# Performance work log

Measured on AMD Instinct MI355X. Metric: run time of the kernel, lower is better.

## Reference

```python
import jax, jax.numpy as jnp
import numpy as np

D_MODEL = 2048
HEADS = 16
HEAD_DIM = D_MODEL // HEADS
INNER = 8192
SEQ = 2048
EPS = 1e-5


def _layernorm(x, g, b):
    mu = jnp.mean(x, axis=-1, keepdims=True)
    var = jnp.mean(jnp.square(x - mu), axis=-1, keepdims=True)
    return (x - mu) * jax.lax.rsqrt(var + EPS) * g + b


def setup_inputs() -> dict:
    key = jax.random.key(0)
    ks = jax.random.split(key, 10)
    s = 0.02
    return {
        "x": jax.random.normal(ks[0], (1, SEQ, D_MODEL), dtype=jnp.float32),
        "C_w": jax.random.normal(ks[1], (D_MODEL, 3 * D_MODEL), dtype=jnp.float32) * s,
        "C_b": jnp.zeros((3 * D_MODEL,), dtype=jnp.float32),
        "lin_w": jax.random.normal(ks[2], (D_MODEL, D_MODEL), dtype=jnp.float32) * s,
        "lin_b": jnp.zeros((D_MODEL,), dtype=jnp.float32),
        "ff1_w": jax.random.normal(ks[3], (D_MODEL, INNER), dtype=jnp.float32) * s,
        "ff1_b": jnp.zeros((INNER,), dtype=jnp.float32),
        "ff2_w": jax.random.normal(ks[4], (INNER, D_MODEL), dtype=jnp.float32) * s,
        "ff2_b": jnp.zeros((D_MODEL,), dtype=jnp.float32),
        "ln1_g": jnp.ones((D_MODEL,), dtype=jnp.float32),
        "ln1_b": jnp.zeros((D_MODEL,), dtype=jnp.float32),
        "ln2_g": jnp.ones((D_MODEL,), dtype=jnp.float32),
        "ln2_b": jnp.zeros((D_MODEL,), dtype=jnp.float32),
    }


def reference(x, C_w, C_b, lin_w, lin_b, ff1_w, ff1_b, ff2_w, ff2_b,
              ln1_g, ln1_b, ln2_g, ln2_b):
    b, s, d = x.shape
    c = x @ C_w + C_b                       # [b, s, 3d]
    q, k, v = jnp.split(c, 3, axis=2)
    q = q.reshape(b, s, HEADS, HEAD_DIM)
    k = k.reshape(b, s, HEADS, HEAD_DIM)
    v = v.reshape(b, s, HEADS, HEAD_DIM)
    # NOTE: source scales by sqrt(d_model), NOT sqrt(head_dim)
    qk = jnp.einsum('bqhd,bkhd->bhqk', q, k) / jnp.sqrt(jnp.float32(d))
    causal = jnp.tril(jnp.ones((s, s), dtype=bool))  # [s, s]
    qk = jnp.where(causal[None, None, :, :], qk, -jnp.inf)
    scores = jax.nn.softmax(qk, axis=3)
    out = jnp.einsum('bhqk,bkhd->bqhd', scores, v).reshape(b, s, d)
    attn = out @ lin_w + lin_b
    h1 = _layernorm(x + attn, ln1_g, ln1_b)
    ff = jax.nn.gelu(h1 @ ff1_w + ff1_b, approximate=False) @ ff2_w + ff2_b
    return _layernorm(h1 + ff, ln2_g, ln2_b)
```

## Files before the change

kernel.cpp:

```cpp
#include <hip/hip_runtime.h>
#include <hip/hip_bf16.h>

#define SEQ 2048
#define DM 2048
#define NH 16
#define HD 128
#define FF 8192

typedef float f4v __attribute__((ext_vector_type(4)));
typedef short s8v __attribute__((ext_vector_type(8)));

__device__ __forceinline__ ushort f2bf(float f) {
  unsigned int x = __float_as_uint(f);
  unsigned int r = (x + 0x7FFFu + ((x >> 16) & 1u)) >> 16;
  return (ushort)r;
}

__global__ __launch_bounds__(256) void k_cvt(const float* __restrict__ in,
                                             ushort* __restrict__ out, int n4) {
  int i = blockIdx.x * 256 + threadIdx.x;
  if (i >= n4) return;
  f4v v = reinterpret_cast<const f4v*>(in)[i];
  ushort4 u;
  u.x = f2bf(v[0]); u.y = f2bf(v[1]); u.z = f2bf(v[2]); u.w = f2bf(v[3]);
  reinterpret_cast<ushort4*>(out)[i] = u;
}

__global__ __launch_bounds__(256) void k_tr(const float* __restrict__ W,
                                            ushort* __restrict__ Wt,
                                            int K, int N) {
  __shared__ float tile[32][33];
  int tx = threadIdx.x & 31, ty = threadIdx.x >> 5;
  int n0 = blockIdx.x * 32, k0 = blockIdx.y * 32;
#pragma unroll
  for (int i = 0; i < 4; ++i)
    tile[ty + i * 8][tx] = W[(size_t)(k0 + ty + i * 8) * N + n0 + tx];
  __syncthreads();
#pragma unroll
  for (int i = 0; i < 4; ++i)
    Wt[(size_t)(n0 + ty + i * 8) * K + k0 + tx] = f2bf(tile[tx][ty + i * 8]);
}

__global__ __launch_bounds__(256) void k_gemm(const ushort* __restrict__ A,
                                              const ushort* __restrict__ Bt,
                                              const float* __restrict__ bias,
                                              float* __restrict__ Cf,
                                              ushort* __restrict__ Cb,
                                              int M, int N, int K, int gelu) {
  __shared__ ushort As[128][72];
  __shared__ ushort Bs[128][72];
  int m0 = blockIdx.y * 128, n0 = blockIdx.x * 128;
  int t = threadIdx.x;
  int wave = t >> 6, lane = t & 63;
  int wm = (wave >> 1) * 64, wn = (wave & 1) * 64;
  int quad = lane >> 4, l16 = lane & 15;
  f4v acc[4][4] = {};
  int srow = t >> 3, scol = (t & 7) * 8;
  for (int k0 = 0; k0 < K; k0 += 64) {
#pragma unroll
    for (int p = 0; p < 4; ++p) {
      int r = srow + p * 32;
      *(uint4*)&As[r][scol] = *(const uint4*)&A[(size_t)(m0 + r) * K + k0 + scol];
      *(uint4*)&Bs[r][scol] = *(const uint4*)&Bt[(size_t)(n0 + r) * K + k0 + scol];
    }
    __syncthreads();
#pragma unroll
    for (int kk = 0; kk < 64; kk += 32) {
      s8v af[4], bf[4];
#pragma unroll
      for (int i = 0; i < 4; ++i)
        af[i] = *(const s8v*)&As[wm + i * 16 + l16][kk + quad * 8];
#pragma unroll
      for (int j = 0; j < 4; ++j)
        bf[j] = *(const s8v*)&Bs[wn + j * 16 + l16][kk + quad * 8];
#pragma unroll
      for (int i = 0; i < 4; ++i)
#pragma unroll
        for (int j = 0; j < 4; ++j)
          acc[i][j] = __builtin_amdgcn_mfma_f32_16x16x32_bf16(af[i], bf[j], acc[i][j], 0, 0, 0);
    }
    __syncthreads();
  }
#pragma unroll
  for (int i = 0; i < 4; ++i) {
    int rbase = m0 + wm + i * 16 + quad * 4;
#pragma unroll
    for (int j = 0; j < 4; ++j) {
      int cidx = n0 + wn + j * 16 + l16;
      float b = bias[cidx];
#pragma unroll
      for (int r = 0; r < 4; ++r) {
        float v = acc[i][j][r] + b;
        if (gelu) v = 0.5f * v * (1.0f + erff(v * 0.70710678118654752f));
        if (Cf) Cf[(size_t)(rbase + r) * N + cidx] = v;
        if (Cb) Cb[(size_t)(rbase + r) * N + cidx] = f2bf(v);
      }
    }
  }
}

__global__ __launch_bounds__(256) void k_attn_mfma(const ushort* __restrict__ qkv,
                                                   ushort* __restrict__ ctx) {
  __shared__ ushort Ks[64][136];
  __shared__ ushort Vt[128][72];
  __shared__ ushort Ps[4][16][72];
  const int idx = blockIdx.x;
  const int h = idx & (NH - 1);
  const int qt = (SEQ / 64 - 1) - (idx >> 4);
  const int q0 = qt * 64;
  const int t = threadIdx.x;
  const int wave = t >> 6, lane = t & 63;
  const int quad = lane >> 4, l16 = lane & 15;
  const float scale = 0.022097086912079608f;

  s8v aq[4];
  {
    const ushort* qp = qkv + (size_t)(q0 + 16 * wave + l16) * (3 * DM) + h * HD + quad * 8;
#pragma unroll
    for (int ks = 0; ks < 4; ++ks)
      aq[ks] = *(const s8v*)(qp + ks * 32);
  }
  f4v acc_o[8] = {};
  float m_r[4], l_r[4];
#pragma unroll
  for (int r = 0; r < 4; ++r) { m_r[r] = -1e30f; l_r[r] = 0.0f; }

  for (int kt = 0; kt <= qt; ++kt) {
    const int k0 = kt * 64;
    __syncthreads();
    {
      const ushort* kp = qkv + (size_t)k0 * (3 * DM) + DM + h * HD;
#pragma unroll
      for (int i = 0; i < 4; ++i) {
        int ch = t + i * 256;
        int row = ch >> 4, c8 = (ch & 15) * 8;
        *(s8v*)&Ks[row][c8] = *(const s8v*)(kp + (size_t)row * (3 * DM) + c8);
      }
      const ushort* vp = qkv + (size_t)k0 * (3 * DM) + 2 * DM + h * HD;
#pragma unroll
      for (int i = 0; i < 4; ++i) {
        int id = t + i * 256;
        int d = id & 127, sg = id >> 7;
        ushort e0 = vp[(size_t)(sg * 8 + 0) * (3 * DM) + d];
        ushort e1 = vp[(size_t)(sg * 8 + 1) * (3 * DM) + d];
        ushort e2 = vp[(size_t)(sg * 8 + 2) * (3 * DM) + d];
        ushort e3 = vp[(size_t)(sg * 8 + 3) * (3 * DM) + d];
        ushort e4 = vp[(size_t)(sg * 8 + 4) * (3 * DM) + d];
        ushort e5 = vp[(size_t)(sg * 8 + 5) * (3 * DM) + d];
        ushort e6 = vp[(size_t)(sg * 8 + 6) * (3 * DM) + d];
        ushort e7 = vp[(size_t)(sg * 8 + 7) * (3 * DM) + d];
        uint4 pk;
        pk.x = (uint)e0 | ((uint)e1 << 16);
        pk.y = (uint)e2 | ((uint)e3 << 16);
        pk.z = (uint)e4 | ((uint)e5 << 16);
        pk.w = (uint)e6 | ((uint)e7 << 16);
        *(uint4*)&Vt[d][sg * 8] = pk;
      }
    }
    __syncthreads();

    f4v sacc[4] = {};
#pragma unroll
    for (int ks = 0; ks < 4; ++ks) {
      s8v bk[4];
#pragma unroll
      for (int j = 0; j < 4; ++j)
        bk[j] = *(const s8v*)&Ks[j * 16 + l16][ks * 32 + quad * 8];
#pragma unroll
      for (int j = 0; j < 4; ++j)
        sacc[j] = __builtin_amdgcn_mfma_f32_16x16x32_bf16(aq[ks], bk[j], sacc[j], 0, 0, 0);
    }
    if (kt == qt) {
#pragma unroll
      for (int j = 0; j < 4; ++j)
#pragma unroll
        for (int r = 0; r < 4; ++r) {
          int lrow = 16 * wave + quad * 4 + r;
          int lcol = j * 16 + l16;
          sacc[j][r] = (lcol > lrow) ? -1e30f : sacc[j][r] * scale;
        }
    } else {
#pragma unroll
      for (int j = 0; j < 4; ++j)
#pragma unroll
        for (int r = 0; r < 4; ++r) sacc[j][r] *= scale;
    }
    float alpha[4];
#pragma unroll
    for (int r = 0; r < 4; ++r) {
      float mx = fmaxf(fmaxf(sacc[0][r], sacc[1][r]), fmaxf(sacc[2][r], sacc[3][r]));
      mx = fmaxf(mx, __shfl_xor(mx, 1));
      mx = fmaxf(mx, __shfl_xor(mx, 2));
      mx = fmaxf(mx, __shfl_xor(mx, 4));
      mx = fmaxf(mx, __shfl_xor(mx, 8));
      float mn = fmaxf(m_r[r], mx);
      alpha[r] = __expf(m_r[r] - mn);
      m_r[r] = mn;
      float ps = 0.0f;
#pragma unroll
      for (int j = 0; j < 4; ++j) {
        float p = __expf(sacc[j][r] - mn);
        sacc[j][r] = p;
        ps += p;
      }
      ps += __shfl_xor(ps, 1);
      ps += __shfl_xor(ps, 2);
      ps += __shfl_xor(ps, 4);
      ps += __shfl_xor(ps, 8);
      l_r[r] = l_r[r] * alpha[r] + ps;
    }
#pragma unroll
    for (int j = 0; j < 4; ++j)
#pragma unroll
      for (int r = 0; r < 4; ++r)
        Ps[wave][quad * 4 + r][j * 16 + l16] = f2bf(sacc[j][r]);
#pragma unroll
    for (int nd = 0; nd < 8; ++nd)
#pragma unroll
      for (int r = 0; r < 4; ++r) acc_o[nd][r] *= alpha[r];
#pragma unroll
    for (int ks2 = 0; ks2 < 2; ++ks2) {
      s8v ap = *(const s8v*)&Ps[wave][l16][ks2 * 32 + quad * 8];
#pragma unroll
      for (int nd = 0; nd < 8; ++nd) {
        s8v bv = *(const s8v*)&Vt[nd * 16 + l16][ks2 * 32 + quad * 8];
        acc_o[nd] = __builtin_amdgcn_mfma_f32_16x16x32_bf16(ap, bv, acc_o[nd], 0, 0, 0);
      }
    }
  }
  float rl[4];
#pragma unroll
  for (int r = 0; r < 4; ++r) rl[r] = 1.0f / l_r[r];
#pragma unroll
  for (int nd = 0; nd < 8; ++nd) {
    int col = h * HD + nd * 16 + l16;
#pragma unroll
    for (int r = 0; r < 4; ++r) {
      int row = q0 + 16 * wave + quad * 4 + r;
      ctx[(size_t)row * DM + col] = f2bf(acc_o[nd][r] * rl[r]);
    }
  }
}

__global__ __launch_bounds__(256) void k_ln(const float* __restrict__ A,
                                            const float* __restrict__ B,
                                            const float* __restrict__ g,
                                            const float* __restrict__ be,
                                            float* __restrict__ outf,
                                            ushort* __restrict__ outb) {
  int row = blockIdx.x;
  int t = threadIdx.x;
  const f4v* av = reinterpret_cast<const f4v*>(A + (size_t)row * DM);
  const f4v* bv = reinterpret_cast<const f4v*>(B + (size_t)row * DM);
  f4v x0 = av[t] + bv[t];
  f4v x1 = av[t + 256] + bv[t + 256];
  float s = x0[0] + x0[1] + x0[2] + x0[3] + x1[0] + x1[1] + x1[2] + x1[3];
  float q = x0[0]*x0[0] + x0[1]*x0[1] + x0[2]*x0[2] + x0[3]*x0[3]
          + x1[0]*x1[0] + x1[1]*x1[1] + x1[2]*x1[2] + x1[3]*x1[3];
#pragma unroll
  for (int off = 32; off; off >>= 1) {
    s += __shfl_down(s, off, 64);
    q += __shfl_down(q, off, 64);
  }
  __shared__ float rs[4], rq[4];
  if ((t & 63) == 0) { rs[t >> 6] = s; rq[t >> 6] = q; }
  __syncthreads();
  s = rs[0] + rs[1] + rs[2] + rs[3];
  q = rq[0] + rq[1] + rq[2] + rq[3];
  float mu = s * (1.0f / DM);
  float var = q * (1.0f / DM) - mu * mu;
  float rstd = rsqrtf(var + 1e-5f);
  const f4v* gv = reinterpret_cast<const f4v*>(g);
  const f4v* bev = reinterpret_cast<const f4v*>(be);
  f4v y0 = (x0 - mu) * rstd * gv[t] + bev[t];
  f4v y1 = (x1 - mu) * rstd * gv[t + 256] + bev[t + 256];
  reinterpret_cast<f4v*>(outf + (size_t)row * DM)[t] = y0;
  reinterpret_cast<f4v*>(outf + (size_t)row * DM)[t + 256] = y1;
  if (outb) {
    ushort4 u0, u1;
    u0.x = f2bf(y0[0]); u0.y = f2bf(y0[1]); u0.z = f2bf(y0[2]); u0.w = f2bf(y0[3]);
    u1.x = f2bf(y1[0]); u1.y = f2bf(y1[1]); u1.z = f2bf(y1[2]); u1.w = f2bf(y1[3]);
    reinterpret_cast<ushort4*>(outb + (size_t)row * DM)[t] = u0;
    reinterpret_cast<ushort4*>(outb + (size_t)row * DM)[t + 256] = u1;
  }
}

extern "C" void kernel_launch(void* const* d_in, const int* in_sizes, int n_in,
                              void* d_out, int out_size, void* d_ws, size_t ws_size,
                              hipStream_t stream) {
  const float* x     = (const float*)d_in[0];
  const float* C_w   = (const float*)d_in[1];
  const float* C_b   = (const float*)d_in[2];
  const float* lin_w = (const float*)d_in[3];
  const float* lin_b = (const float*)d_in[4];
  const float* ff1_w = (const float*)d_in[5];
  const float* ff1_b = (const float*)d_in[6];
  const float* ff2_w = (const float*)d_in[7];
  const float* ff2_b = (const float*)d_in[8];
  const float* ln1g  = (const float*)d_in[9];
  const float* ln1b  = (const float*)d_in[10];
  const float* ln2g  = (const float*)d_in[11];
  const float* ln2b  = (const float*)d_in[12];

  char* ws = (char*)d_ws;
  size_t off = 0;
  auto take = [&](size_t bytes) {
    char* p = ws + off;
    off += (bytes + 255) & ~(size_t)255;
    return p;
  };
  ushort* Wt   = (ushort*)take((size_t)FF * DM * 2);
  ushort* qkvb = (ushort*)take((size_t)SEQ * 3 * DM * 2);
  ushort* xb   = (ushort*)take((size_t)SEQ * DM * 2);
  ushort* ctxb = (ushort*)take((size_t)SEQ * DM * 2);
  ushort* bigb = (ushort*)take((size_t)SEQ * FF * 2);
  float*  attn = (float*) take((size_t)SEQ * DM * 4);
  float*  h1   = (float*) take((size_t)SEQ * DM * 4);
  float*  ff2o = (float*) take((size_t)SEQ * DM * 4);

  k_cvt<<<SEQ * DM / 1024, 256, 0, stream>>>(x, xb, SEQ * DM / 4);
  k_tr<<<dim3(3 * DM / 32, DM / 32), 256, 0, stream>>>(C_w, Wt, DM, 3 * DM);
  k_gemm<<<dim3(3 * DM / 128, SEQ / 128), 256, 0, stream>>>(xb, Wt, C_b, nullptr, qkvb, SEQ, 3 * DM, DM, 0);
  k_attn_mfma<<<dim3((SEQ / 64) * NH), 256, 0, stream>>>(qkvb, ctxb);
  k_tr<<<dim3(DM / 32, DM / 32), 256, 0, stream>>>(lin_w, Wt, DM, DM);
  k_gemm<<<dim3(DM / 128, SEQ / 128), 256, 0, stream>>>(ctxb, Wt, lin_b, attn, nullptr, SEQ, DM, DM, 0);
  k_ln<<<SEQ, 256, 0, stream>>>(x, attn, ln1g, ln1b, h1, xb);
  k_tr<<<dim3(FF / 32, DM / 32), 256, 0, stream>>>(ff1_w, Wt, DM, FF);
  k_gemm<<<dim3(FF / 128, SEQ / 128), 256, 0, stream>>>(xb, Wt, ff1_b, nullptr, bigb, SEQ, FF, DM, 1);
  k_tr<<<dim3(DM / 32, FF / 32), 256, 0, stream>>>(ff2_w, Wt, FF, DM);
  k_gemm<<<dim3(DM / 128, SEQ / 128), 256, 0, stream>>>(bigb, Wt, ff2_b, ff2o, nullptr, SEQ, DM, FF, 0);
  k_ln<<<SEQ, 256, 0, stream>>>(h1, ff2o, ln2g, ln2b, (float*)d_out, (ushort*)nullptr);
}
```

Measured before the change: 710.4 us.

## Use direct global-to-LDS loads with XOR swizzle in GEMM; vectorize transpose

The GEMM tile staging now uses global_load_lds so data goes from global memory straight into LDS without passing through registers. Padding is replaced by an XOR swizzle on column groups so the fragment reads avoid bank conflicts. The weight transpose kernel now does float4 loads and ushort4 stores instead of scalar ones. Correctness depends on the per-wave LDS destination layout of the builtin matching the swizzled addressing, and there is still no double buffering.

```diff
diff --git a/kernel.cpp b/kernel.cpp
--- a/kernel.cpp
+++ b/kernel.cpp
@@ -14,6 +14,12 @@
   unsigned int x = __float_as_uint(f);
   unsigned int r = (x + 0x7FFFu + ((x >> 16) & 1u)) >> 16;
   return (ushort)r;
+}
+
+#define AS1 __attribute__((address_space(1)))
+#define AS3 __attribute__((address_space(3)))
+__device__ __forceinline__ void load16_lds(const ushort* g, ushort* l) {
+  __builtin_amdgcn_global_load_lds((const AS1 unsigned int*)g, (AS3 unsigned int*)l, 16, 0, 0);
 }
 
 __global__ __launch_bounds__(256) void k_cvt(const float* __restrict__ in,
@@ -29,16 +35,19 @@
 __global__ __launch_bounds__(256) void k_tr(const float* __restrict__ W,
                                             ushort* __restrict__ Wt,
                                             int K, int N) {
-  __shared__ float tile[32][33];
-  int tx = threadIdx.x & 31, ty = threadIdx.x >> 5;
+  __shared__ float tile[32][36];
+  int t = threadIdx.x;
   int n0 = blockIdx.x * 32, k0 = blockIdx.y * 32;
-#pragma unroll
-  for (int i = 0; i < 4; ++i)
-    tile[ty + i * 8][tx] = W[(size_t)(k0 + ty + i * 8) * N + n0 + tx];
+  int lr = t >> 3, lc = (t & 7) * 4;
+  *(f4v*)&tile[lr][lc] = *(const f4v*)&W[(size_t)(k0 + lr) * N + n0 + lc];
   __syncthreads();
-#pragma unroll
-  for (int i = 0; i < 4; ++i)
-    Wt[(size_t)(n0 + ty + i * 8) * K + k0 + tx] = f2bf(tile[tx][ty + i * 8]);
+  int sn = t >> 3, sk = (t & 7) * 4;
+  ushort4 u;
+  u.x = f2bf(tile[sk + 0][sn]);
+  u.y = f2bf(tile[sk + 1][sn]);
+  u.z = f2bf(tile[sk + 2][sn]);
+  u.w = f2bf(tile[sk + 3][sn]);
+  *(ushort4*)&Wt[(size_t)(n0 + sn) * K + k0 + sk] = u;
 }
 
 __global__ __launch_bounds__(256) void k_gemm(const ushort* __restrict__ A,
@@ -47,32 +56,42 @@
                                               float* __restrict__ Cf,
                                               ushort* __restrict__ Cb,
                                               int M, int N, int K, int gelu) {
-  __shared__ ushort As[128][72];
-  __shared__ ushort Bs[128][72];
-  int m0 = blockIdx.y * 128, n0 = blockIdx.x * 128;
-  int t = threadIdx.x;
-  int wave = t >> 6, lane = t & 63;
-  int wm = (wave >> 1) * 64, wn = (wave & 1) * 64;
-  int quad = lane >> 4, l16 = lane & 15;
+  __shared__ ushort As[128 * 64];
+  __shared__ ushort Bs[128 * 64];
+  const int m0 = blockIdx.y * 128, n0 = blockIdx.x * 128;
+  const int t = threadIdx.x;
+  const int wave = t >> 6, lane = t & 63;
+  const int wm = (wave >> 1) * 64, wn = (wave & 1) * 64;
+  const int quad = lane >> 4, l16 = lane & 15;
   f4v acc[4][4] = {};
-  int srow = t >> 3, scol = (t & 7) * 8;
+  const int srow = lane >> 3;
+  const int scg = (lane & 7) ^ srow;
+  const ushort* gA = A + (size_t)(m0 + wave * 32 + srow) * K + scg * 8;
+  const ushort* gB = Bt + (size_t)(n0 + wave * 32 + srow) * K + scg * 8;
+  ushort* lA = &As[(wave * 32 + srow - srow) * 64];
+  ushort* lB = &Bs[(wave * 32) * 64];
+  lA = &As[(wave * 32) * 64];
+
   for (int k0 = 0; k0 < K; k0 += 64) {
 #pragma unroll
     for (int p = 0; p < 4; ++p) {
-      int r = srow + p * 32;
-      *(uint4*)&As[r][scol] = *(const uint4*)&A[(size_t)(m0 + r) * K + k0 + scol];
-      *(uint4*)&Bs[r][scol] = *(const uint4*)&Bt[(size_t)(n0 + r) * K + k0 + scol];
+      load16_lds(gA + (size_t)p * 8 * K + k0, lA + p * 8 * 64);
+      load16_lds(gB + (size_t)p * 8 * K + k0, lB + p * 8 * 64);
     }
     __syncthreads();
 #pragma unroll
     for (int kk = 0; kk < 64; kk += 32) {
       s8v af[4], bf[4];
 #pragma unroll
-      for (int i = 0; i < 4; ++i)
-        af[i] = *(const s8v*)&As[wm + i * 16 + l16][kk + quad * 8];
-#pragma unroll
-      for (int j = 0; j < 4; ++j)
-        bf[j] = *(const s8v*)&Bs[wn + j * 16 + l16][kk + quad * 8];
+      for (int i = 0; i < 4; ++i) {
+        int ar = wm + i * 16 + l16;
+        af[i] = *(const s8v*)&As[ar * 64 + ((((kk >> 3) + quad) ^ (ar & 7)) * 8)];
+      }
+#pragma unroll
+      for (int j = 0; j < 4; ++j) {
+        int br = wn + j * 16 + l16;
+        bf[j] = *(const s8v*)&Bs[br * 64 + ((((kk >> 3) + quad) ^ (br & 7)) * 8)];
+      }
 #pragma unroll
       for (int i = 0; i < 4; ++i)
 #pragma unroll
```

Result: no change. 718.2 us (+1.1%).
